# Optimization experiments

Hardware: AMD Instinct MI355X
Metric: run time of the kernel (lower is better)

The kernel has to match this reference:

```python
import jax, jax.numpy as jnp
import numpy as np

H = 16          # num_heads
EPS = 1e-6      # RMSNorm eps


def setup_inputs() -> dict:
    key = jax.random.key(0)
    ks = jax.random.split(key, 5)
    B, N, D = 4, 4096, 1024
    x = jax.random.normal(ks[0], (B, N, D), dtype=jnp.float32)
    q = jax.random.normal(ks[1], (D,), dtype=jnp.float32)
    k = jax.random.normal(ks[2], (D,), dtype=jnp.float32)
    log_decay = jax.random.normal(ks[3], (H,), dtype=jnp.float32)
    norm_weight = jnp.ones((D,), dtype=jnp.float32)
    o_w = jax.random.normal(ks[4], (D, D), dtype=jnp.float32) * 0.02
    return {"x": x, "q": q, "k": k, "log_decay": log_decay,
            "norm_weight": norm_weight, "o_w": o_w}


def reference(x, q, k, log_decay, norm_weight, o_w):
    b, n, dm = x.shape
    dh = dm // H
    qh = q.reshape(H, dh)            # per-head query vector (constant over b, n)
    kh = k.reshape(H, dh)            # per-head key vector
    v = x.reshape(b, n, H, dh)       # values = input tokens
    # exp(logsigmoid(a)) == sigmoid(a): per-head decay in (0, 1)
    lam = jax.nn.sigmoid(log_decay)  # (H,)

    def step(S, v_t):
        # S: (b, H, dh, dh) recurrent state;  v_t: (b, H, dh)
        S = lam[None, :, None, None] * S + kh[None, :, :, None] * v_t[:, :, None, :]
        o_t = jnp.einsum('hd,bhdv->bhv', qh, S)
        return S, o_t

    S0 = jnp.zeros((b, H, dh, dh), dtype=x.dtype)
    _, o = jax.lax.scan(step, S0, jnp.moveaxis(v, 1, 0))  # o: (n, b, H, dh)
    o = jnp.moveaxis(o, 0, 1).reshape(b, n, dm)

    # RMSNorm over the channel dim
    o = o * jax.lax.rsqrt(jnp.mean(o * o, axis=-1, keepdims=True) + EPS) * norm_weight
    # o_proj (no bias)
    return o @ o_w.T
```

## Files before the change

kernel.cpp:

```cpp
#include <hip/hip_runtime.h>
#include <hip/hip_bf16.h>
#include <cstdint>
#include <cstddef>

#define HH   16
#define BB   4
#define NN   4096
#define DD   1024
#define MM   (BB * NN)
#define NC   128
#define LC   32
#define EPSV 1e-6f

typedef short short8 __attribute__((ext_vector_type(8)));
typedef float floatx4 __attribute__((ext_vector_type(4)));

__device__ __forceinline__ void async_copy16(const void* g, void* l) {
    __builtin_amdgcn_global_load_lds(
        (const __attribute__((address_space(1))) void*)g,
        (__attribute__((address_space(3))) void*)l, 16, 0, 0);
}

__device__ __forceinline__ uint2 pack_bf16x4(float a, float b, float c, float d) {
    union { __hip_bfloat16 h[4]; uint2 u; } cv;
    cv.h[0] = __float2bfloat16(a); cv.h[1] = __float2bfloat16(b);
    cv.h[2] = __float2bfloat16(c); cv.h[3] = __float2bfloat16(d);
    return cv.u;
}

__global__ void k_meta(const float* __restrict__ q, const float* __restrict__ k,
                       const float* __restrict__ ld, float* __restrict__ meta) {
    int tid = threadIdx.x;
    float p = q[tid] * k[tid];
    #pragma unroll
    for (int off = 32; off > 0; off >>= 1) p += __shfl_xor(p, off);
    if ((tid & 63) == 0) meta[16 + (tid >> 6)] = p;
    if (tid < HH) meta[tid] = 1.f / (1.f + expf(-ld[tid]));
}

__global__ void k_wconv(const float* __restrict__ ow, const float* __restrict__ nw,
                        __hip_bfloat16* __restrict__ wp) {
    size_t i4 = (size_t)blockIdx.x * 256 + threadIdx.x;
    int j = (int)((i4 * 4) & (DD - 1));
    float4 v = ((const float4*)ow)[i4];
    ((uint2*)wp)[i4] = pack_bf16x4(v.x * nw[j], v.y * nw[j + 1],
                                   v.z * nw[j + 2], v.w * nw[j + 3]);
}

__global__ void k_chunk_end(const float* __restrict__ x, const float* __restrict__ meta,
                            float* __restrict__ E) {
    int b = blockIdx.x >> 7, c = blockIdx.x & (NC - 1);
    int j4 = threadIdx.x;
    float lam = meta[(j4 * 4) >> 6];
    const float4* xp = (const float4*)(x + ((size_t)(b * NN + c * LC)) * DD) + j4;
    float4 e = {0.f, 0.f, 0.f, 0.f};
    #pragma unroll
    for (int t = 0; t < LC; ++t) {
        float4 v = xp[(size_t)t * (DD / 4)];
        e.x = fmaf(lam, e.x, v.x); e.y = fmaf(lam, e.y, v.y);
        e.z = fmaf(lam, e.z, v.z); e.w = fmaf(lam, e.w, v.w);
    }
    ((float4*)(E + (size_t)blockIdx.x * DD))[j4] = e;
}

__global__ void k_carry(const float* __restrict__ meta, const float* __restrict__ E,
                        float* __restrict__ P) {
    __shared__ float tile[NC][33];
    int b = blockIdx.x >> 5, jg = blockIdx.x & 31;
    int tid = threadIdx.x;
    int cc = tid >> 5, jj = tid & 31;
    #pragma unroll
    for (int it = 0; it < 16; ++it) {
        int c = it * 8 + cc;
        tile[c][jj] = E[(size_t)(b * NC + c) * DD + jg * 32 + jj];
    }
    __syncthreads();
    if (tid < 32) {
        int j = jg * 32 + tid;
        float lam = meta[j >> 6];
        float lamL = lam;
        lamL *= lamL; lamL *= lamL; lamL *= lamL; lamL *= lamL; lamL *= lamL;
        float p = 0.f;
        for (int c = 0; c < NC; ++c) {
            float e = tile[c][tid];
            tile[c][tid] = p;
            p = fmaf(lamL, p, e);
        }
    }
    __syncthreads();
    #pragma unroll
    for (int it = 0; it < 16; ++it) {
        int c = it * 8 + cc;
        P[(size_t)(b * NC + c) * DD + jg * 32 + jj] = tile[c][jj];
    }
}

__global__ void k_scan(const float* __restrict__ x, const float* __restrict__ meta,
                       const float* __restrict__ P, __hip_bfloat16* __restrict__ obf,
                       float* __restrict__ sumsq) {
    int b = blockIdx.x >> 7, c = blockIdx.x & (NC - 1);
    int j4 = threadIdx.x;
    int h = (j4 * 4) >> 6;
    float lam = meta[h];
    float ch  = meta[16 + h];
    int row0 = b * NN + c * LC;
    const float4* xp = (const float4*)(x + (size_t)row0 * DD) + j4;
    float4 y = ((const float4*)(P + (size_t)blockIdx.x * DD))[j4];
    int lane0 = ((threadIdx.x & 63) == 0);
    for (int t = 0; t < LC; ++t) {
        float4 v = xp[(size_t)t * (DD / 4)];
        y.x = fmaf(lam, y.x, v.x); y.y = fmaf(lam, y.y, v.y);
        y.z = fmaf(lam, y.z, v.z); y.w = fmaf(lam, y.w, v.w);
        float ox = ch * y.x, oy = ch * y.y, oz = ch * y.z, ow = ch * y.w;
        ((uint2*)(obf + (size_t)(row0 + t) * DD))[j4] = pack_bf16x4(ox, oy, oz, ow);
        float s = ox * ox + oy * oy + oz * oz + ow * ow;
        #pragma unroll
        for (int off = 32; off > 0; off >>= 1) s += __shfl_xor(s, off);
        if (lane0) atomicAdd(&sumsq[row0 + t], s);
    }
}

__launch_bounds__(256)
__global__ void k_gemm(const __hip_bfloat16* __restrict__ A,
                       const __hip_bfloat16* __restrict__ W,
                       const float* __restrict__ sumsq, float* __restrict__ out) {
    __shared__ __attribute__((aligned(16))) short sA[128 * 64];
    __shared__ __attribute__((aligned(16))) short sB[128 * 64];
    const int tid = threadIdx.x;
    const int l = tid & 63, w = tid >> 6;
    const int wm = w >> 1, wn = w & 1;
    const int g = blockIdx.x;
    const int bm = g & 127, bn = g >> 7;
    const int m0 = bm * 128, n0 = bn * 128;
    const short* Ag = (const short*)A;
    const short* Wg = (const short*)W;

    floatx4 acc[4][4] = {};

    int srow[4], scol[4];
    #pragma unroll
    for (int i = 0; i < 4; ++i) {
        int s = i * 256 + tid;
        srow[i] = s >> 3;
        scol[i] = ((s & 7) ^ ((s >> 3) & 7)) * 8;
    }

    for (int kt = 0; kt < 16; ++kt) {
        const int k0 = kt * 64;
        #pragma unroll
        for (int i = 0; i < 4; ++i) {
            async_copy16(Ag + (size_t)(m0 + srow[i]) * 1024 + k0 + scol[i],
                         (char*)sA + i * 4096 + w * 1024);
            async_copy16(Wg + (size_t)(n0 + srow[i]) * 1024 + k0 + scol[i],
                         (char*)sB + i * 4096 + w * 1024);
        }
        __syncthreads();
        #pragma unroll
        for (int ks = 0; ks < 2; ++ks) {
            short8 af[4], bf[4];
            #pragma unroll
            for (int mt = 0; mt < 4; ++mt) {
                int row = wm * 64 + mt * 16 + (l & 15);
                int c8  = (ks * 4 + (l >> 4)) ^ (row & 7);
                af[mt] = *(const short8*)(sA + row * 64 + c8 * 8);
            }
            #pragma unroll
            for (int nt = 0; nt < 4; ++nt) {
                int row = wn * 64 + nt * 16 + (l & 15);
                int c8  = (ks * 4 + (l >> 4)) ^ (row & 7);
                bf[nt] = *(const short8*)(sB + row * 64 + c8 * 8);
            }
            #pragma unroll
            for (int mt = 0; mt < 4; ++mt)
                #pragma unroll
                for (int nt = 0; nt < 4; ++nt)
                    acc[mt][nt] = __builtin_amdgcn_mfma_f32_16x16x32_bf16(af[mt], bf[nt], acc[mt][nt], 0, 0, 0);
        }
        __syncthreads();
    }

    #pragma unroll
    for (int mt = 0; mt < 4; ++mt) {
        #pragma unroll
        for (int r = 0; r < 4; ++r) {
            int mrow = m0 + wm * 64 + mt * 16 + (l >> 4) * 4 + r;
            float rs = rsqrtf(sumsq[mrow] * (1.f / 1024.f) + EPSV);
            #pragma unroll
            for (int nt = 0; nt < 4; ++nt) {
                int col = n0 + wn * 64 + nt * 16 + (l & 15);
                out[(size_t)mrow * 1024 + col] = acc[mt][nt][r] * rs;
            }
        }
    }
}

extern "C" void kernel_launch(void* const* d_in, const int* in_sizes, int n_in,
                              void* d_out, int out_size, void* d_ws, size_t ws_size,
                              hipStream_t stream) {
    const float* x  = (const float*)d_in[0];
    const float* q  = (const float*)d_in[1];
    const float* k  = (const float*)d_in[2];
    const float* ld = (const float*)d_in[3];
    const float* nw = (const float*)d_in[4];
    const float* ow = (const float*)d_in[5];
    float* out = (float*)d_out;

    char* ws = (char*)d_ws;
    float* meta  = (float*)(ws + 0);
    float* sumsq = (float*)(ws + 256);
    float* E     = (float*)(ws + 65792);
    float* P     = (float*)(ws + 2162944);
    __hip_bfloat16* Wp  = (__hip_bfloat16*)(ws + 4260096);
    __hip_bfloat16* Obf = (__hip_bfloat16*)(ws + 6357248);

    hipMemsetAsync(sumsq, 0, MM * sizeof(float), stream);
    k_meta<<<1, 1024, 0, stream>>>(q, k, ld, meta);
    k_wconv<<<(DD * DD / 4) / 256, 256, 0, stream>>>(ow, nw, Wp);
    k_chunk_end<<<BB * NC, 256, 0, stream>>>(x, meta, E);
    k_carry<<<BB * 32, 256, 0, stream>>>(meta, E, P);
    k_scan<<<BB * NC, 256, 0, stream>>>(x, meta, P, Obf, sumsq);
    k_gemm<<<(MM / 128) * (DD / 128), 256, 0, stream>>>(Obf, Wp, sumsq, out);
}
```

Before: 190.2 us.

## Double-buffer GEMM with 256x256 tiles, XCD-aware mapping, and atomic-free row sums

The GEMM now uses 256x256 output tiles with 512 threads and a double-buffered LDS pipeline. It splits each 64-wide K step into two halves, issues the async loads for the next stage while MFMAs run on the current one, raises wave priority around the MFMA bursts, and remaps blocks so each XCD handles neighbouring M rows. The scan kernel reduces per-row sum of squares through shared memory and writes the result once instead of using atomics, which also removes the memset. Larger tiles add register pressure (128 accumulator floats per thread) and leave only 256 blocks, which may underfill the CUs.

```diff
diff --git a/kernel.cpp b/kernel.cpp
--- a/kernel.cpp
+++ b/kernel.cpp
@@ -98,15 +98,16 @@
 __global__ void k_scan(const float* __restrict__ x, const float* __restrict__ meta,
                        const float* __restrict__ P, __hip_bfloat16* __restrict__ obf,
                        float* __restrict__ sumsq) {
+    __shared__ float ssq[4][LC];
     int b = blockIdx.x >> 7, c = blockIdx.x & (NC - 1);
     int j4 = threadIdx.x;
     int h = (j4 * 4) >> 6;
     float lam = meta[h];
     float ch  = meta[16 + h];
     int row0 = b * NN + c * LC;
+    int lane = threadIdx.x & 63, w = threadIdx.x >> 6;
     const float4* xp = (const float4*)(x + (size_t)row0 * DD) + j4;
     float4 y = ((const float4*)(P + (size_t)blockIdx.x * DD))[j4];
-    int lane0 = ((threadIdx.x & 63) == 0);
     for (int t = 0; t < LC; ++t) {
         float4 v = xp[(size_t)t * (DD / 4)];
         y.x = fmaf(lam, y.x, v.x); y.y = fmaf(lam, y.y, v.y);
@@ -116,78 +117,97 @@
         float s = ox * ox + oy * oy + oz * oz + ow * ow;
         #pragma unroll
         for (int off = 32; off > 0; off >>= 1) s += __shfl_xor(s, off);
-        if (lane0) atomicAdd(&sumsq[row0 + t], s);
-    }
-}
-
-__launch_bounds__(256)
+        if (lane == 0) ssq[w][t] = s;
+    }
+    __syncthreads();
+    if (threadIdx.x < LC) {
+        int t = threadIdx.x;
+        sumsq[row0 + t] = ssq[0][t] + ssq[1][t] + ssq[2][t] + ssq[3][t];
+    }
+}
+
+#define GEMM_STAGE(BUF, MAT, KK, TN)                                           \
+  do {                                                                         \
+    const short* _src = (MAT) ? Wg : Ag;                                       \
+    const int _b0 = (MAT) ? n0 : m0;                                           \
+    char* _dst = (char*)&lds[BUF][MAT][KK][0] + w * 1024;                      \
+    _Pragma("unroll") for (int _i = 0; _i < 2; ++_i)                           \
+      async_copy16(_src + (size_t)(_b0 + _i * 128 + rr) * 1024                 \
+                        + (TN) * 64 + (KK) * 32 + oo * 8,                      \
+                   _dst + _i * 8192);                                          \
+  } while (0)
+
+#define GEMM_REGION(BUF, KK)                                                   \
+  do {                                                                         \
+    short8 af[8]; short8 bf[4];                                                \
+    _Pragma("unroll") for (int mt = 0; mt < 8; ++mt)                           \
+      af[mt] = *(const short8*)(&lds[BUF][0][KK][0] +                          \
+                                (arow_base + mt * 16) * 32 + p_rd * 8);        \
+    _Pragma("unroll") for (int nt = 0; nt < 4; ++nt)                           \
+      bf[nt] = *(const short8*)(&lds[BUF][1][KK][0] +                          \
+                                (brow_base + nt * 16) * 32 + p_rd * 8);        \
+    __builtin_amdgcn_s_setprio(1);                                             \
+    _Pragma("unroll") for (int mt = 0; mt < 8; ++mt) {                         \
+      _Pragma("unroll") for (int nt = 0; nt < 4; ++nt)                         \
+        acc[mt][nt] = __builtin_amdgcn_mfma_f32_16x16x32_bf16(                 \
+            af[mt], bf[nt], acc[mt][nt], 0, 0, 0);                             \
+    }                                                                          \
+    __builtin_amdgcn_s_setprio(0);                                             \
+  } while (0)
+
+__launch_bounds__(512, 2)
 __global__ void k_gemm(const __hip_bfloat16* __restrict__ A,
                        const __hip_bfloat16* __restrict__ W,
                        const float* __restrict__ sumsq, float* __restrict__ out) {
-    __shared__ __attribute__((aligned(16))) short sA[128 * 64];
-    __shared__ __attribute__((aligned(16))) short sB[128 * 64];
+    __shared__ __attribute__((aligned(16))) short lds[2][2][2][256 * 32];
     const int tid = threadIdx.x;
-    const int l = tid & 63, w = tid >> 6;
-    const int wm = w >> 1, wn = w & 1;
+    const int lane = tid & 63, w = tid >> 6;
+    const int wm = w >> 2, wn = w & 3;
     const int g = blockIdx.x;
-    const int bm = g & 127, bn = g >> 7;
-    const int m0 = bm * 128, n0 = bn * 128;
+    const int xcd = g & 7, idx = g >> 3;
+    const int bm = xcd * 8 + (idx >> 2);
+    const int bn = idx & 3;
+    const int m0 = bm * 256, n0 = bn * 256;
     const short* Ag = (const short*)A;
     const short* Wg = (const short*)W;
 
-    floatx4 acc[4][4] = {};
-
-    int srow[4], scol[4];
-    #pragma unroll
-    for (int i = 0; i < 4; ++i) {
-        int s = i * 256 + tid;
-        srow[i] = s >> 3;
-        scol[i] = ((s & 7) ^ ((s >> 3) & 7)) * 8;
-    }
-
-    for (int kt = 0; kt < 16; ++kt) {
-        const int k0 = kt * 64;
-        #pragma unroll
-        for (int i = 0; i < 4; ++i) {
-            async_copy16(Ag + (size_t)(m0 + srow[i]) * 1024 + k0 + scol[i],
-                         (char*)sA + i * 4096 + w * 1024);
-            async_copy16(Wg + (size_t)(n0 + srow[i]) * 1024 + k0 + scol[i],
-                         (char*)sB + i * 4096 + w * 1024);
+    const int rr = tid >> 2;
+    const int oo = (tid & 3) ^ ((rr >> 1) & 3);
+
+    const int p_rd = (lane >> 4) ^ (((lane & 15) >> 1) & 3);
+    const int arow_base = wm * 128 + (lane & 15);
+    const int brow_base = wn * 64 + (lane & 15);
+
+    floatx4 acc[8][4] = {};
+
+    GEMM_STAGE(0, 0, 0, 0); GEMM_STAGE(0, 1, 0, 0);
+    GEMM_STAGE(0, 0, 1, 0); GEMM_STAGE(0, 1, 1, 0);
+
+    for (int t = 0; t < 16; ++t) {
+        const int buf = t & 1;
+        asm volatile("s_waitcnt vmcnt(4)" ::: "memory");
+        __builtin_amdgcn_s_barrier();
+        if (t < 15) { GEMM_STAGE(buf ^ 1, 0, 0, t + 1); GEMM_STAGE(buf ^ 1, 1, 0, t + 1); }
+        GEMM_REGION(buf, 0);
+        if (t < 15) {
+            asm volatile("s_waitcnt vmcnt(4)" ::: "memory");
+        } else {
+            asm volatile("s_waitcnt vmcnt(0)" ::: "memory");
         }
-        __syncthreads();
-        #pragma unroll
-        for (int ks = 0; ks < 2; ++ks) {
-            short8 af[4], bf[4];
-            #pragma unroll
-            for (int mt = 0; mt < 4; ++mt) {
-                int row = wm * 64 + mt * 16 + (l & 15);
-                int c8  = (ks * 4 + (l >> 4)) ^ (row & 7);
-                af[mt] = *(const short8*)(sA + row * 64 + c8 * 8);
-            }
-            #pragma unroll
-            for (int nt = 0; nt < 4; ++nt) {
-                int row = wn * 64 + nt * 16 + (l & 15);
-                int c8  = (ks * 4 + (l >> 4)) ^ (row & 7);
-                bf[nt] = *(const short8*)(sB + row * 64 + c8 * 8);
-            }
-            #pragma unroll
-            for (int mt = 0; mt < 4; ++mt)
-                #pragma unroll
-                for (int nt = 0; nt < 4; ++nt)
-                    acc[mt][nt] = __builtin_amdgcn_mfma_f32_16x16x32_bf16(af[mt], bf[nt], acc[mt][nt], 0, 0, 0);
-        }
-        __syncthreads();
-    }
-
-    #pragma unroll
-    for (int mt = 0; mt < 4; ++mt) {
+        __builtin_amdgcn_s_barrier();
+        if (t < 15) { GEMM_STAGE(buf ^ 1, 0, 1, t + 1); GEMM_STAGE(buf ^ 1, 1, 1, t + 1); }
+        GEMM_REGION(buf, 1);
+    }
+
+    #pragma unroll
+    for (int mt = 0; mt < 8; ++mt) {
         #pragma unroll
         for (int r = 0; r < 4; ++r) {
-            int mrow = m0 + wm * 64 + mt * 16 + (l >> 4) * 4 + r;
+            int mrow = m0 + wm * 128 + mt * 16 + (lane >> 4) * 4 + r;
             float rs = rsqrtf(sumsq[mrow] * (1.f / 1024.f) + EPSV);
             #pragma unroll
             for (int nt = 0; nt < 4; ++nt) {
-                int col = n0 + wn * 64 + nt * 16 + (l & 15);
+                int col = n0 + wn * 64 + nt * 16 + (lane & 15);
                 out[(size_t)mrow * 1024 + col] = acc[mt][nt][r] * rs;
             }
         }
@@ -213,11 +233,10 @@
     __hip_bfloat16* Wp  = (__hip_bfloat16*)(ws + 4260096);
     __hip_bfloat16* Obf = (__hip_bfloat16*)(ws + 6357248);
 
-    hipMemsetAsync(sumsq, 0, MM * sizeof(float), stream);
     k_meta<<<1, 1024, 0, stream>>>(q, k, ld, meta);
     k_wconv<<<(DD * DD / 4) / 256, 256, 0, stream>>>(ow, nw, Wp);
     k_chunk_end<<<BB * NC, 256, 0, stream>>>(x, meta, E);
     k_carry<<<BB * 32, 256, 0, stream>>>(meta, E, P);
     k_scan<<<BB * NC, 256, 0, stream>>>(x, meta, P, Obf, sumsq);
-    k_gemm<<<(MM / 128) * (DD / 128), 256, 0, stream>>>(Obf, Wp, sumsq, out);
-}
+    k_gemm<<<(MM / 256) * (DD / 256), 512, 0, stream>>>(Obf, Wp, sumsq, out);
+}
```

Measured after the change: 176.3 us. 7.3% less time.
